# Optimization experiments

Hardware: AMD Instinct MI355X
Metric: run time of the kernel (lower is better)

Reference implementation:

```python
import jax, jax.numpy as jnp
import numpy as np

N_NODES = 50000
N_EDGES = 800000
D_FEAT = 128


def setup_inputs() -> dict:
    key = jax.random.key(0)
    k1, k2, k3 = jax.random.split(key, 3)
    x = jax.random.normal(k1, (N_NODES, D_FEAT), dtype=jnp.float32)
    edge_index = jax.random.randint(k2, (2, N_EDGES), 0, N_NODES, dtype=jnp.int64)
    eps = jnp.zeros((1,), dtype=jnp.float32)  # trainable eps, init 0
    p = jax.random.uniform(k3, (1,), dtype=jnp.float32, minval=-1.0, maxval=1.0)
    return {"x": x, "edge_index": edge_index, "eps": eps, "p": p}


def reference(x, edge_index, eps, p):
    # x: [N, d]; edge_index: [2, E] with (row, col)
    row, col = edge_index[0], edge_index[1]
    n = x.shape[0]

    # symmetric-ish GCN norm (degree computed over col only, as in source)
    deg = jax.ops.segment_sum(jnp.ones_like(col, dtype=x.dtype), col, num_segments=n)
    deg_inv_sqrt = jnp.where(deg > 0, deg ** -0.5, 0.0)
    norm = deg_inv_sqrt[row] * deg_inv_sqrt[col]  # [E]

    # nonlinear aggregation branch
    pp = jax.nn.sigmoid(p) * 2.0  # scalar in (0, 2)
    scale = pp * x  # [N, d]
    softmax = jnp.exp(scale - scale.max())  # global-max-stabilized exp

    sm_col = softmax[col]  # [E, d] gather
    deg_div = jax.ops.segment_sum(sm_col * norm[:, None], row, num_segments=n)  # [N, d]
    weights = sm_col / (deg_div[row] + 1e-6)  # [E, d]

    agg = jax.ops.segment_sum(weights * x[col] * norm[:, None], row, num_segments=n)  # [N, d]
    out = agg + (1.0 + eps) * x
    return out
```

## Files before the change

### kernel.cpp

```cpp
#include <hip/hip_runtime.h>
#include <hip/hip_fp16.h>
#include <math.h>

#define N_NODES 50000
#define N_EDGES 800000
#define D_FEAT 128

#define BSHIFT 6
#define BNODES 64
#define NBUCK ((N_NODES + BNODES - 1) / BNODES)
#define BCAP 1280
#define SLOT_CAP 64

#define PART_BLOCKS 256
#define PART_CHUNK (N_EDGES / PART_BLOCKS)

typedef __attribute__((ext_vector_type(4))) _Float16 half4;

__global__ void __launch_bounds__(256) k_cvtmax(const float* __restrict__ x,
                                                half4* __restrict__ x16,
                                                float* __restrict__ partials) {
    const float4* x4 = (const float4*)x;
    const int total4 = N_NODES * D_FEAT / 4;
    float m = -INFINITY;
    for (int i = blockIdx.x * blockDim.x + threadIdx.x; i < total4; i += gridDim.x * blockDim.x) {
        float4 v = x4[i];
        m = fmaxf(m, fmaxf(fmaxf(v.x, v.y), fmaxf(v.z, v.w)));
        half4 h;
        h.x = (_Float16)v.x; h.y = (_Float16)v.y; h.z = (_Float16)v.z; h.w = (_Float16)v.w;
        x16[i] = h;
    }
    for (int off = 32; off > 0; off >>= 1)
        m = fmaxf(m, __shfl_down(m, off, 64));
    __shared__ float smem[4];
    int lane = threadIdx.x & 63, wid = threadIdx.x >> 6;
    if (lane == 0) smem[wid] = m;
    __syncthreads();
    if (threadIdx.x == 0)
        partials[blockIdx.x] = fmaxf(fmaxf(smem[0], smem[1]), fmaxf(smem[2], smem[3]));
}

__global__ void __launch_bounds__(256) k_max2(const float* __restrict__ partials,
                                              float* __restrict__ maxval) {
    float m = fmaxf(partials[threadIdx.x], partials[threadIdx.x + 256]);
    for (int off = 32; off > 0; off >>= 1)
        m = fmaxf(m, __shfl_down(m, off, 64));
    __shared__ float smem[4];
    int lane = threadIdx.x & 63, wid = threadIdx.x >> 6;
    if (lane == 0) smem[wid] = m;
    __syncthreads();
    if (threadIdx.x == 0)
        maxval[0] = fmaxf(fmaxf(smem[0], smem[1]), fmaxf(smem[2], smem[3]));
}

__global__ void __launch_bounds__(512) k_part(const int* __restrict__ row,
                                              const int* __restrict__ col,
                                              int* __restrict__ gcur_row,
                                              int* __restrict__ gcur_col,
                                              int2* __restrict__ be_row,
                                              int* __restrict__ be_col) {
    __shared__ int h_row[NBUCK];
    __shared__ int h_col[NBUCK];
    int e0 = blockIdx.x * PART_CHUNK;
    for (int i = threadIdx.x; i < NBUCK; i += 512) { h_row[i] = 0; h_col[i] = 0; }
    __syncthreads();
    for (int e = e0 + threadIdx.x; e < e0 + PART_CHUNK; e += 512) {
        atomicAdd(&h_row[row[e] >> BSHIFT], 1);
        atomicAdd(&h_col[col[e] >> BSHIFT], 1);
    }
    __syncthreads();
    for (int i = threadIdx.x; i < NBUCK; i += 512) {
        int base_r = atomicAdd(&gcur_row[i], h_row[i]);
        h_row[i] = i * BCAP + base_r;
        int base_c = atomicAdd(&gcur_col[i], h_col[i]);
        h_col[i] = i * BCAP + base_c;
    }
    __syncthreads();
    for (int e = e0 + threadIdx.x; e < e0 + PART_CHUNK; e += 512) {
        int r = row[e], c = col[e];
        int pr = atomicAdd(&h_row[r >> BSHIFT], 1);
        if (pr < (r >> BSHIFT) * BCAP + BCAP) be_row[pr] = make_int2(r, c);
        int pc = atomicAdd(&h_col[c >> BSHIFT], 1);
        if (pc < (c >> BSHIFT) * BCAP + BCAP) be_col[pc] = c;
    }
}

__global__ void __launch_bounds__(256) k_degcol(const int* __restrict__ gcur_col,
                                                const int* __restrict__ be_col,
                                                float* __restrict__ dis) {
    __shared__ int h[BNODES];
    int b = blockIdx.x;
    if (threadIdx.x < BNODES) h[threadIdx.x] = 0;
    __syncthreads();
    int cnt = min(gcur_col[b], BCAP);
    int base = b * BCAP;
    for (int k = threadIdx.x; k < cnt; k += 256)
        atomicAdd(&h[be_col[base + k] & (BNODES - 1)], 1);
    __syncthreads();
    if (threadIdx.x < BNODES) {
        int n = (b << BSHIFT) + threadIdx.x;
        if (n < N_NODES) {
            int d = h[threadIdx.x];
            dis[n] = (d > 0) ? rsqrtf((float)d) : 0.0f;
        }
    }
}

__global__ void __launch_bounds__(512) k_agg(const half4* __restrict__ x16,
                                             const float* __restrict__ x,
                                             const int* __restrict__ gcur_row,
                                             const int2* __restrict__ be_row,
                                             const float* __restrict__ dis,
                                             const float* __restrict__ maxval,
                                             const float* __restrict__ eps_p,
                                             const float* __restrict__ p_p,
                                             float* __restrict__ out) {
    __shared__ int s_cnt[BNODES];
    __shared__ int s_slot[BNODES][SLOT_CAP];
    __shared__ float s_dis[BNODES][SLOT_CAP];
    int b = blockIdx.x;
    if (threadIdx.x < BNODES) s_cnt[threadIdx.x] = 0;
    __syncthreads();
    int ecnt = min(gcur_row[b], BCAP);
    int base = b * BCAP;
    for (int k = threadIdx.x; k < ecnt; k += 512) {
        int2 e = be_row[base + k];
        int ln = e.x & (BNODES - 1);
        int pos = atomicAdd(&s_cnt[ln], 1);
        if (pos < SLOT_CAP) {
            s_slot[ln][pos] = e.y;
            s_dis[ln][pos] = dis[e.y];
        }
    }
    __syncthreads();

    int g = threadIdx.x >> 5;
    int t = threadIdx.x & 31;
    float pp = 2.0f / (1.0f + __expf(-p_p[0]));
    float M  = pp * maxval[0];
    float ke = 1.0f + eps_p[0];
    const float4* x4 = (const float4*)x;

    for (int ln = g; ln < BNODES; ln += 16) {
        int n = (b << BSHIFT) + ln;
        if (n >= N_NODES) continue;
        int cnt = min(s_cnt[ln], SLOT_CAP);
        float dn = dis[n];
        float4 S = make_float4(0.f, 0.f, 0.f, 0.f);
        float4 T = make_float4(0.f, 0.f, 0.f, 0.f);
        #pragma unroll 4
        for (int j = 0; j < cnt; ++j) {
            int c = s_slot[ln][j];
            float nr = dn * s_dis[ln][j];
            half4 hv = x16[c * 32 + t];
            float x0 = (float)hv.x, x1 = (float)hv.y, x2 = (float)hv.z, x3 = (float)hv.w;
            float e0 = __expf(fmaf(pp, x0, -M));
            float e1 = __expf(fmaf(pp, x1, -M));
            float e2 = __expf(fmaf(pp, x2, -M));
            float e3 = __expf(fmaf(pp, x3, -M));
            float w0 = nr * e0, w1 = nr * e1, w2 = nr * e2, w3 = nr * e3;
            S.x += w0; S.y += w1; S.z += w2; S.w += w3;
            T.x = fmaf(w0, x0, T.x);
            T.y = fmaf(w1, x1, T.y);
            T.z = fmaf(w2, x2, T.z);
            T.w = fmaf(w3, x3, T.w);
        }
        float4 xn = x4[n * 32 + t];
        float4 o;
        o.x = T.x / (S.x + 1e-6f) + ke * xn.x;
        o.y = T.y / (S.y + 1e-6f) + ke * xn.y;
        o.z = T.z / (S.z + 1e-6f) + ke * xn.z;
        o.w = T.w / (S.w + 1e-6f) + ke * xn.w;
        ((float4*)out)[n * 32 + t] = o;
    }
}

extern "C" void kernel_launch(void* const* d_in, const int* in_sizes, int n_in,
                              void* d_out, int out_size, void* d_ws, size_t ws_size,
                              hipStream_t stream) {
    const float* x   = (const float*)d_in[0];
    const int*   ei  = (const int*)d_in[1];
    const float* eps = (const float*)d_in[2];
    const float* p   = (const float*)d_in[3];
    float* out = (float*)d_out;

    const int* row = ei;
    const int* col = ei + N_EDGES;

    char* ws = (char*)d_ws;
    int*   gcur_row = (int*)ws;
    int*   gcur_col = (int*)(ws + 4 * NBUCK);
    float* maxval   = (float*)(ws + 4 * 2 * NBUCK);
    float* partials = (float*)(ws + 4 * (2 * NBUCK + 1));
    float* dis      = (float*)(ws + 4 * (2 * NBUCK + 1 + 512));
    size_t off = 4 * (size_t)(2 * NBUCK + 1 + 512 + N_NODES);
    off = (off + 15) & ~(size_t)15;
    half4* x16      = (half4*)(ws + off);
    off += (size_t)N_NODES * D_FEAT * 2;
    int*   be_col   = (int*)(ws + off);
    off += (size_t)NBUCK * BCAP * 4;
    int2*  be_row   = (int2*)(ws + off);

    hipMemsetAsync(ws, 0, 4 * 2 * NBUCK, stream);

    k_cvtmax<<<512, 256, 0, stream>>>(x, x16, partials);
    k_max2<<<1, 256, 0, stream>>>(partials, maxval);
    k_part<<<PART_BLOCKS, 512, 0, stream>>>(row, col, gcur_row, gcur_col, be_row, be_col);
    k_degcol<<<NBUCK, 256, 0, stream>>>(gcur_col, be_col, dis);
    k_agg<<<NBUCK, 512, 0, stream>>>(x16, x, gcur_row, be_row, dis, maxval, eps, p, out);
}
```

Measured before the change: 169.3 us.

## Fuse all stages into one persistent cooperative kernel with grid syncs

Replaces the memset and five separate launches with a single cooperative persistent kernel. It runs convert/max, edge partitioning, column degree and aggregation as phases separated by grid.sync, with blocks looping over buckets. Counter zeroing and the final max reduction move inside the kernel. The exponent is rewritten as exp2f with log2(e) folded into the scale and max constants. This removes launch gaps and the memset, at the cost of grid-wide barriers and a grid capped at 512 blocks, which gives uneven bucket distribution in the aggregation phase. A three-kernel fallback is kept, but it zeroes the counters in the same kernel that accumulates into them, without a grid-wide barrier between the two.

```diff
diff --git a/kernel.cpp b/kernel.cpp
--- a/kernel.cpp
+++ b/kernel.cpp
@@ -1,4 +1,5 @@
 #include <hip/hip_runtime.h>
+#include <hip/hip_cooperative_groups.h>
 #include <hip/hip_fp16.h>
 #include <math.h>
 
@@ -12,71 +13,79 @@
 #define BCAP 1280
 #define SLOT_CAP 64
 
-#define PART_BLOCKS 256
-#define PART_CHUNK (N_EDGES / PART_BLOCKS)
+#define BLOCK 512
+#define MAXGRID 512
+#define PREP_GRID 512
 
 typedef __attribute__((ext_vector_type(4))) _Float16 half4;
-
-__global__ void __launch_bounds__(256) k_cvtmax(const float* __restrict__ x,
-                                                half4* __restrict__ x16,
-                                                float* __restrict__ partials) {
+namespace cg = cooperative_groups;
+
+struct SmemLayout {
+    int   cnt[BNODES];
+    float scal[4];
+    int   slot[BNODES][SLOT_CAP];
+    float dsv[BNODES][SLOT_CAP];
+};
+
+__device__ __forceinline__ void phase_cvtmax(const float* __restrict__ x,
+                                             half4* __restrict__ x16,
+                                             float* __restrict__ partials,
+                                             int* __restrict__ gcur,
+                                             SmemLayout& sm) {
+    const int tid = threadIdx.x;
+    const int gtid = blockIdx.x * BLOCK + tid;
+    if (gtid < 2 * NBUCK) gcur[gtid] = 0;
     const float4* x4 = (const float4*)x;
     const int total4 = N_NODES * D_FEAT / 4;
+    const int stride = gridDim.x * BLOCK;
     float m = -INFINITY;
-    for (int i = blockIdx.x * blockDim.x + threadIdx.x; i < total4; i += gridDim.x * blockDim.x) {
+    for (int i = gtid; i < total4; i += stride) {
         float4 v = x4[i];
         m = fmaxf(m, fmaxf(fmaxf(v.x, v.y), fmaxf(v.z, v.w)));
         half4 h;
-        h.x = (_Float16)v.x; h.y = (_Float16)v.y; h.z = (_Float16)v.z; h.w = (_Float16)v.w;
+        h.x = (_Float16)v.x; h.y = (_Float16)v.y;
+        h.z = (_Float16)v.z; h.w = (_Float16)v.w;
         x16[i] = h;
     }
     for (int off = 32; off > 0; off >>= 1)
         m = fmaxf(m, __shfl_down(m, off, 64));
-    __shared__ float smem[4];
-    int lane = threadIdx.x & 63, wid = threadIdx.x >> 6;
-    if (lane == 0) smem[wid] = m;
-    __syncthreads();
-    if (threadIdx.x == 0)
-        partials[blockIdx.x] = fmaxf(fmaxf(smem[0], smem[1]), fmaxf(smem[2], smem[3]));
-}
-
-__global__ void __launch_bounds__(256) k_max2(const float* __restrict__ partials,
-                                              float* __restrict__ maxval) {
-    float m = fmaxf(partials[threadIdx.x], partials[threadIdx.x + 256]);
-    for (int off = 32; off > 0; off >>= 1)
-        m = fmaxf(m, __shfl_down(m, off, 64));
-    __shared__ float smem[4];
-    int lane = threadIdx.x & 63, wid = threadIdx.x >> 6;
-    if (lane == 0) smem[wid] = m;
-    __syncthreads();
-    if (threadIdx.x == 0)
-        maxval[0] = fmaxf(fmaxf(smem[0], smem[1]), fmaxf(smem[2], smem[3]));
-}
-
-__global__ void __launch_bounds__(512) k_part(const int* __restrict__ row,
-                                              const int* __restrict__ col,
-                                              int* __restrict__ gcur_row,
-                                              int* __restrict__ gcur_col,
-                                              int2* __restrict__ be_row,
-                                              int* __restrict__ be_col) {
-    __shared__ int h_row[NBUCK];
-    __shared__ int h_col[NBUCK];
-    int e0 = blockIdx.x * PART_CHUNK;
-    for (int i = threadIdx.x; i < NBUCK; i += 512) { h_row[i] = 0; h_col[i] = 0; }
-    __syncthreads();
-    for (int e = e0 + threadIdx.x; e < e0 + PART_CHUNK; e += 512) {
+    float* red = (float*)sm.cnt;
+    const int lane = tid & 63, wid = tid >> 6;
+    if (lane == 0) red[wid] = m;
+    __syncthreads();
+    if (tid == 0) {
+        for (int w = 1; w < BLOCK / 64; ++w) m = fmaxf(m, red[w]);
+        partials[blockIdx.x] = m;
+    }
+    __syncthreads();
+}
+
+__device__ __forceinline__ void phase_part(const int* __restrict__ row,
+                                           const int* __restrict__ col,
+                                           int* __restrict__ gcur,
+                                           int2* __restrict__ be_row,
+                                           int* __restrict__ be_col,
+                                           SmemLayout& sm) {
+    int* h_row = (int*)sm.slot;
+    int* h_col = (int*)sm.dsv;
+    const int tid = threadIdx.x;
+    const int G = gridDim.x;
+    const int echunk = (N_EDGES + G - 1) / G;
+    const int e0 = blockIdx.x * echunk;
+    const int e1 = min(e0 + echunk, N_EDGES);
+    for (int i = tid; i < NBUCK; i += BLOCK) { h_row[i] = 0; h_col[i] = 0; }
+    __syncthreads();
+    for (int e = e0 + tid; e < e1; e += BLOCK) {
         atomicAdd(&h_row[row[e] >> BSHIFT], 1);
         atomicAdd(&h_col[col[e] >> BSHIFT], 1);
     }
     __syncthreads();
-    for (int i = threadIdx.x; i < NBUCK; i += 512) {
-        int base_r = atomicAdd(&gcur_row[i], h_row[i]);
-        h_row[i] = i * BCAP + base_r;
-        int base_c = atomicAdd(&gcur_col[i], h_col[i]);
-        h_col[i] = i * BCAP + base_c;
-    }
-    __syncthreads();
-    for (int e = e0 + threadIdx.x; e < e0 + PART_CHUNK; e += 512) {
+    for (int i = tid; i < NBUCK; i += BLOCK) {
+        h_row[i] = i * BCAP + atomicAdd(&gcur[i], h_row[i]);
+        h_col[i] = i * BCAP + atomicAdd(&gcur[NBUCK + i], h_col[i]);
+    }
+    __syncthreads();
+    for (int e = e0 + tid; e < e1; e += BLOCK) {
         int r = row[e], c = col[e];
         int pr = atomicAdd(&h_row[r >> BSHIFT], 1);
         if (pr < (r >> BSHIFT) * BCAP + BCAP) be_row[pr] = make_int2(r, c);
@@ -85,94 +94,174 @@
     }
 }
 
-__global__ void __launch_bounds__(256) k_degcol(const int* __restrict__ gcur_col,
-                                                const int* __restrict__ be_col,
-                                                float* __restrict__ dis) {
-    __shared__ int h[BNODES];
-    int b = blockIdx.x;
-    if (threadIdx.x < BNODES) h[threadIdx.x] = 0;
-    __syncthreads();
-    int cnt = min(gcur_col[b], BCAP);
-    int base = b * BCAP;
-    for (int k = threadIdx.x; k < cnt; k += 256)
-        atomicAdd(&h[be_col[base + k] & (BNODES - 1)], 1);
-    __syncthreads();
-    if (threadIdx.x < BNODES) {
-        int n = (b << BSHIFT) + threadIdx.x;
-        if (n < N_NODES) {
-            int d = h[threadIdx.x];
-            dis[n] = (d > 0) ? rsqrtf((float)d) : 0.0f;
+__device__ __forceinline__ void phase_degcol(const int* __restrict__ gcur,
+                                             const int* __restrict__ be_col,
+                                             float* __restrict__ dis,
+                                             SmemLayout& sm) {
+    const int tid = threadIdx.x;
+    for (int b = blockIdx.x; b < NBUCK; b += gridDim.x) {
+        if (tid < BNODES) sm.cnt[tid] = 0;
+        __syncthreads();
+        int cnt = min(gcur[NBUCK + b], BCAP);
+        int base = b * BCAP;
+        for (int k = tid; k < cnt; k += BLOCK)
+            atomicAdd(&sm.cnt[be_col[base + k] & (BNODES - 1)], 1);
+        __syncthreads();
+        if (tid < BNODES) {
+            int n = (b << BSHIFT) + tid;
+            if (n < N_NODES) {
+                int d0 = sm.cnt[tid];
+                dis[n] = (d0 > 0) ? rsqrtf((float)d0) : 0.0f;
+            }
         }
-    }
-}
-
-__global__ void __launch_bounds__(512) k_agg(const half4* __restrict__ x16,
-                                             const float* __restrict__ x,
-                                             const int* __restrict__ gcur_row,
-                                             const int2* __restrict__ be_row,
-                                             const float* __restrict__ dis,
-                                             const float* __restrict__ maxval,
-                                             const float* __restrict__ eps_p,
-                                             const float* __restrict__ p_p,
-                                             float* __restrict__ out) {
-    __shared__ int s_cnt[BNODES];
-    __shared__ int s_slot[BNODES][SLOT_CAP];
-    __shared__ float s_dis[BNODES][SLOT_CAP];
-    int b = blockIdx.x;
-    if (threadIdx.x < BNODES) s_cnt[threadIdx.x] = 0;
-    __syncthreads();
-    int ecnt = min(gcur_row[b], BCAP);
-    int base = b * BCAP;
-    for (int k = threadIdx.x; k < ecnt; k += 512) {
-        int2 e = be_row[base + k];
-        int ln = e.x & (BNODES - 1);
-        int pos = atomicAdd(&s_cnt[ln], 1);
-        if (pos < SLOT_CAP) {
-            s_slot[ln][pos] = e.y;
-            s_dis[ln][pos] = dis[e.y];
+        __syncthreads();
+    }
+}
+
+__device__ __forceinline__ void phase_scal(const float* __restrict__ partials,
+                                           int nparts,
+                                           const float* __restrict__ eps_p,
+                                           const float* __restrict__ p_p,
+                                           SmemLayout& sm) {
+    const int tid = threadIdx.x;
+    float m = (tid < nparts) ? partials[tid] : -INFINITY;
+    for (int off = 32; off > 0; off >>= 1)
+        m = fmaxf(m, __shfl_down(m, off, 64));
+    float* red = (float*)sm.cnt;
+    const int lane = tid & 63, wid = tid >> 6;
+    if (lane == 0) red[wid] = m;
+    __syncthreads();
+    if (tid == 0) {
+        for (int w = 1; w < BLOCK / 64; ++w) m = fmaxf(m, red[w]);
+        float pp = 2.0f / (1.0f + __expf(-p_p[0]));
+        const float LOG2E = 1.44269504f;
+        sm.scal[0] = pp * m * LOG2E;
+        sm.scal[1] = pp * LOG2E;
+        sm.scal[2] = 1.0f + eps_p[0];
+    }
+    __syncthreads();
+}
+
+__device__ __forceinline__ void phase_agg(const float* __restrict__ x,
+                                          const half4* __restrict__ x16,
+                                          const int* __restrict__ gcur,
+                                          const int2* __restrict__ be_row,
+                                          const float* __restrict__ dis,
+                                          float* __restrict__ out,
+                                          SmemLayout& sm) {
+    const int tid = threadIdx.x;
+    const float Mlg = sm.scal[0], ppl = sm.scal[1], ke = sm.scal[2];
+    const float4* x4 = (const float4*)x;
+    for (int b = blockIdx.x; b < NBUCK; b += gridDim.x) {
+        if (tid < BNODES) sm.cnt[tid] = 0;
+        __syncthreads();
+        int ecnt = min(gcur[b], BCAP);
+        int base = b * BCAP;
+        for (int k = tid; k < ecnt; k += BLOCK) {
+            int2 e = be_row[base + k];
+            int ln = e.x & (BNODES - 1);
+            int pos = atomicAdd(&sm.cnt[ln], 1);
+            if (pos < SLOT_CAP) {
+                sm.slot[ln][pos] = e.y;
+                sm.dsv[ln][pos] = dis[e.y];
+            }
         }
-    }
-    __syncthreads();
-
-    int g = threadIdx.x >> 5;
-    int t = threadIdx.x & 31;
-    float pp = 2.0f / (1.0f + __expf(-p_p[0]));
-    float M  = pp * maxval[0];
-    float ke = 1.0f + eps_p[0];
-    const float4* x4 = (const float4*)x;
-
-    for (int ln = g; ln < BNODES; ln += 16) {
-        int n = (b << BSHIFT) + ln;
-        if (n >= N_NODES) continue;
-        int cnt = min(s_cnt[ln], SLOT_CAP);
-        float dn = dis[n];
-        float4 S = make_float4(0.f, 0.f, 0.f, 0.f);
-        float4 T = make_float4(0.f, 0.f, 0.f, 0.f);
-        #pragma unroll 4
-        for (int j = 0; j < cnt; ++j) {
-            int c = s_slot[ln][j];
-            float nr = dn * s_dis[ln][j];
-            half4 hv = x16[c * 32 + t];
-            float x0 = (float)hv.x, x1 = (float)hv.y, x2 = (float)hv.z, x3 = (float)hv.w;
-            float e0 = __expf(fmaf(pp, x0, -M));
-            float e1 = __expf(fmaf(pp, x1, -M));
-            float e2 = __expf(fmaf(pp, x2, -M));
-            float e3 = __expf(fmaf(pp, x3, -M));
-            float w0 = nr * e0, w1 = nr * e1, w2 = nr * e2, w3 = nr * e3;
-            S.x += w0; S.y += w1; S.z += w2; S.w += w3;
-            T.x = fmaf(w0, x0, T.x);
-            T.y = fmaf(w1, x1, T.y);
-            T.z = fmaf(w2, x2, T.z);
-            T.w = fmaf(w3, x3, T.w);
+        __syncthreads();
+        int g = tid >> 5;
+        int t = tid & 31;
+        for (int ln = g; ln < BNODES; ln += 16) {
+            int n = (b << BSHIFT) + ln;
+            if (n >= N_NODES) continue;
+            int cnt = min(sm.cnt[ln], SLOT_CAP);
+            float dn = dis[n];
+            float4 S = make_float4(0.f, 0.f, 0.f, 0.f);
+            float4 T = make_float4(0.f, 0.f, 0.f, 0.f);
+            #pragma unroll 4
+            for (int j = 0; j < cnt; ++j) {
+                int c = sm.slot[ln][j];
+                float nr = dn * sm.dsv[ln][j];
+                half4 hv = x16[c * 32 + t];
+                float x0 = (float)hv.x, x1 = (float)hv.y;
+                float x2 = (float)hv.z, x3 = (float)hv.w;
+                float e0 = exp2f(fmaf(ppl, x0, -Mlg));
+                float e1 = exp2f(fmaf(ppl, x1, -Mlg));
+                float e2 = exp2f(fmaf(ppl, x2, -Mlg));
+                float e3 = exp2f(fmaf(ppl, x3, -Mlg));
+                float w0 = nr * e0, w1 = nr * e1, w2 = nr * e2, w3 = nr * e3;
+                S.x += w0; S.y += w1; S.z += w2; S.w += w3;
+                T.x = fmaf(w0, x0, T.x);
+                T.y = fmaf(w1, x1, T.y);
+                T.z = fmaf(w2, x2, T.z);
+                T.w = fmaf(w3, x3, T.w);
+            }
+            float4 xn = x4[n * 32 + t];
+            float4 o;
+            o.x = T.x / (S.x + 1e-6f) + ke * xn.x;
+            o.y = T.y / (S.y + 1e-6f) + ke * xn.y;
+            o.z = T.z / (S.z + 1e-6f) + ke * xn.z;
+            o.w = T.w / (S.w + 1e-6f) + ke * xn.w;
+            ((float4*)out)[n * 32 + t] = o;
         }
-        float4 xn = x4[n * 32 + t];
-        float4 o;
-        o.x = T.x / (S.x + 1e-6f) + ke * xn.x;
-        o.y = T.y / (S.y + 1e-6f) + ke * xn.y;
-        o.z = T.z / (S.z + 1e-6f) + ke * xn.z;
-        o.w = T.w / (S.w + 1e-6f) + ke * xn.w;
-        ((float4*)out)[n * 32 + t] = o;
-    }
+        __syncthreads();
+    }
+}
+
+__global__ void __launch_bounds__(BLOCK, 4) k_fused(
+    const float* __restrict__ x,
+    const int* __restrict__ row,
+    const int* __restrict__ col,
+    const float* __restrict__ eps_p,
+    const float* __restrict__ p_p,
+    float* __restrict__ out,
+    half4* __restrict__ x16,
+    float* __restrict__ partials,
+    int* __restrict__ gcur,
+    int2* __restrict__ be_row,
+    int* __restrict__ be_col,
+    float* __restrict__ dis)
+{
+    cg::grid_group grid = cg::this_grid();
+    __shared__ SmemLayout sm;
+    phase_cvtmax(x, x16, partials, gcur, sm);
+    grid.sync();
+    phase_part(row, col, gcur, be_row, be_col, sm);
+    grid.sync();
+    phase_degcol(gcur, be_col, dis, sm);
+    grid.sync();
+    phase_scal(partials, gridDim.x, eps_p, p_p, sm);
+    phase_agg(x, x16, gcur, be_row, dis, out, sm);
+}
+
+__global__ void __launch_bounds__(BLOCK) k_prep(
+    const float* __restrict__ x, const int* __restrict__ row,
+    const int* __restrict__ col, half4* __restrict__ x16,
+    float* __restrict__ partials, int* __restrict__ gcur,
+    int2* __restrict__ be_row, int* __restrict__ be_col)
+{
+    __shared__ SmemLayout sm;
+    phase_cvtmax(x, x16, partials, gcur, sm);
+    __syncthreads();
+    phase_part(row, col, gcur, be_row, be_col, sm);
+}
+
+__global__ void __launch_bounds__(BLOCK) k_deg(
+    const int* __restrict__ gcur, const int* __restrict__ be_col,
+    float* __restrict__ dis)
+{
+    __shared__ SmemLayout sm;
+    phase_degcol(gcur, be_col, dis, sm);
+}
+
+__global__ void __launch_bounds__(BLOCK) k_aggk(
+    const float* __restrict__ x, const half4* __restrict__ x16,
+    const float* __restrict__ partials, int nparts,
+    const float* __restrict__ eps_p, const float* __restrict__ p_p,
+    const int* __restrict__ gcur, const int2* __restrict__ be_row,
+    const float* __restrict__ dis, float* __restrict__ out)
+{
+    __shared__ SmemLayout sm;
+    phase_scal(partials, nparts, eps_p, p_p, sm);
+    phase_agg(x, x16, gcur, be_row, dis, out, sm);
 }
 
 extern "C" void kernel_launch(void* const* d_in, const int* in_sizes, int n_in,
@@ -188,12 +277,10 @@
     const int* col = ei + N_EDGES;
 
     char* ws = (char*)d_ws;
-    int*   gcur_row = (int*)ws;
-    int*   gcur_col = (int*)(ws + 4 * NBUCK);
-    float* maxval   = (float*)(ws + 4 * 2 * NBUCK);
-    float* partials = (float*)(ws + 4 * (2 * NBUCK + 1));
-    float* dis      = (float*)(ws + 4 * (2 * NBUCK + 1 + 512));
-    size_t off = 4 * (size_t)(2 * NBUCK + 1 + 512 + N_NODES);
+    int*   gcur     = (int*)ws;
+    float* partials = (float*)(ws + 4 * 2 * NBUCK);
+    float* dis      = (float*)(ws + 4 * (2 * NBUCK + MAXGRID));
+    size_t off = 4 * (size_t)(2 * NBUCK + MAXGRID + N_NODES);
     off = (off + 15) & ~(size_t)15;
     half4* x16      = (half4*)(ws + off);
     off += (size_t)N_NODES * D_FEAT * 2;
@@ -201,11 +288,24 @@
     off += (size_t)NBUCK * BCAP * 4;
     int2*  be_row   = (int2*)(ws + off);
 
-    hipMemsetAsync(ws, 0, 4 * 2 * NBUCK, stream);
-
-    k_cvtmax<<<512, 256, 0, stream>>>(x, x16, partials);
-    k_max2<<<1, 256, 0, stream>>>(partials, maxval);
-    k_part<<<PART_BLOCKS, 512, 0, stream>>>(row, col, gcur_row, gcur_col, be_row, be_col);
-    k_degcol<<<NBUCK, 256, 0, stream>>>(gcur_col, be_col, dis);
-    k_agg<<<NBUCK, 512, 0, stream>>>(x16, x, gcur_row, be_row, dis, maxval, eps, p, out);
-}
+    int maxB = 0;
+    hipError_t oe = hipOccupancyMaxActiveBlocksPerMultiprocessor(&maxB, k_fused, BLOCK, 0);
+    bool coop_done = false;
+    if (oe == hipSuccess && maxB > 0) {
+        int g = maxB * 256;
+        if (g > MAXGRID) g = MAXGRID;
+        void* args[] = { (void*)&x, (void*)&row, (void*)&col, (void*)&eps, (void*)&p,
+                         (void*)&out, (void*)&x16, (void*)&partials, (void*)&gcur,
+                         (void*)&be_row, (void*)&be_col, (void*)&dis };
+        hipError_t le = hipLaunchCooperativeKernel((const void*)k_fused, dim3(g),
+                                                   dim3(BLOCK), args, 0, stream);
+        coop_done = (le == hipSuccess);
+    }
+    if (!coop_done) {
+        k_prep<<<PREP_GRID, BLOCK, 0, stream>>>(x, row, col, x16, partials, gcur,
+                                                be_row, be_col);
+        k_deg<<<NBUCK, BLOCK, 0, stream>>>(gcur, be_col, dis);
+        k_aggk<<<NBUCK, BLOCK, 0, stream>>>(x, x16, partials, PREP_GRID, eps, p,
+                                            gcur, be_row, dis, out);
+    }
+}
```

New measurement: 327.3 us. 93.3% more time.

## Fuse conversion/max into partition kernel, fold max reduction into aggregation, shrink buckets

Applied to the files above, without the earlier changes.

Merges the fp16 conversion and max-partial kernel with the edge partition kernel, and moves the final max reduction into each aggregation block. This removes two kernel launches. Bucket size drops from 64 to 32 nodes with 256-thread aggregation blocks and a higher occupancy hint, giving more, smaller blocks. The exponential is rewritten as exp2f with log2e prescaled. The trade-offs are redundant per-block max reduction and more buckets in the shared histograms of the partition phase.

```diff
diff --git a/kernel.cpp b/kernel.cpp
--- a/kernel.cpp
+++ b/kernel.cpp
@@ -6,77 +6,67 @@
 #define N_EDGES 800000
 #define D_FEAT 128
 
-#define BSHIFT 6
-#define BNODES 64
+#define BSHIFT 5
+#define BNODES 32
 #define NBUCK ((N_NODES + BNODES - 1) / BNODES)
-#define BCAP 1280
+#define BCAP 704
 #define SLOT_CAP 64
 
-#define PART_BLOCKS 256
-#define PART_CHUNK (N_EDGES / PART_BLOCKS)
+#define PREP_GRID 256
+#define PREP_BLOCK 512
+#define PREP_CHUNK (N_EDGES / PREP_GRID)
+#define AGG_BLOCK 256
 
 typedef __attribute__((ext_vector_type(4))) _Float16 half4;
 
-__global__ void __launch_bounds__(256) k_cvtmax(const float* __restrict__ x,
-                                                half4* __restrict__ x16,
-                                                float* __restrict__ partials) {
-    const float4* x4 = (const float4*)x;
-    const int total4 = N_NODES * D_FEAT / 4;
-    float m = -INFINITY;
-    for (int i = blockIdx.x * blockDim.x + threadIdx.x; i < total4; i += gridDim.x * blockDim.x) {
-        float4 v = x4[i];
-        m = fmaxf(m, fmaxf(fmaxf(v.x, v.y), fmaxf(v.z, v.w)));
-        half4 h;
-        h.x = (_Float16)v.x; h.y = (_Float16)v.y; h.z = (_Float16)v.z; h.w = (_Float16)v.w;
-        x16[i] = h;
-    }
-    for (int off = 32; off > 0; off >>= 1)
-        m = fmaxf(m, __shfl_down(m, off, 64));
-    __shared__ float smem[4];
-    int lane = threadIdx.x & 63, wid = threadIdx.x >> 6;
-    if (lane == 0) smem[wid] = m;
-    __syncthreads();
-    if (threadIdx.x == 0)
-        partials[blockIdx.x] = fmaxf(fmaxf(smem[0], smem[1]), fmaxf(smem[2], smem[3]));
-}
-
-__global__ void __launch_bounds__(256) k_max2(const float* __restrict__ partials,
-                                              float* __restrict__ maxval) {
-    float m = fmaxf(partials[threadIdx.x], partials[threadIdx.x + 256]);
-    for (int off = 32; off > 0; off >>= 1)
-        m = fmaxf(m, __shfl_down(m, off, 64));
-    __shared__ float smem[4];
-    int lane = threadIdx.x & 63, wid = threadIdx.x >> 6;
-    if (lane == 0) smem[wid] = m;
-    __syncthreads();
-    if (threadIdx.x == 0)
-        maxval[0] = fmaxf(fmaxf(smem[0], smem[1]), fmaxf(smem[2], smem[3]));
-}
-
-__global__ void __launch_bounds__(512) k_part(const int* __restrict__ row,
-                                              const int* __restrict__ col,
-                                              int* __restrict__ gcur_row,
-                                              int* __restrict__ gcur_col,
-                                              int2* __restrict__ be_row,
-                                              int* __restrict__ be_col) {
+__global__ void __launch_bounds__(PREP_BLOCK) k_prep(
+    const float* __restrict__ x, const int* __restrict__ row,
+    const int* __restrict__ col, half4* __restrict__ x16,
+    float* __restrict__ partials, int* __restrict__ gcur,
+    int2* __restrict__ be_row, int* __restrict__ be_col)
+{
     __shared__ int h_row[NBUCK];
     __shared__ int h_col[NBUCK];
-    int e0 = blockIdx.x * PART_CHUNK;
-    for (int i = threadIdx.x; i < NBUCK; i += 512) { h_row[i] = 0; h_col[i] = 0; }
-    __syncthreads();
-    for (int e = e0 + threadIdx.x; e < e0 + PART_CHUNK; e += 512) {
+    __shared__ float red[PREP_BLOCK / 64];
+    const int tid = threadIdx.x;
+
+    {
+        const float4* x4 = (const float4*)x;
+        const int total4 = N_NODES * D_FEAT / 4;
+        float m = -INFINITY;
+        for (int i = blockIdx.x * PREP_BLOCK + tid; i < total4; i += PREP_GRID * PREP_BLOCK) {
+            float4 v = x4[i];
+            m = fmaxf(m, fmaxf(fmaxf(v.x, v.y), fmaxf(v.z, v.w)));
+            half4 h;
+            h.x = (_Float16)v.x; h.y = (_Float16)v.y;
+            h.z = (_Float16)v.z; h.w = (_Float16)v.w;
+            x16[i] = h;
+        }
+        for (int off = 32; off > 0; off >>= 1)
+            m = fmaxf(m, __shfl_down(m, off, 64));
+        if ((tid & 63) == 0) red[tid >> 6] = m;
+        __syncthreads();
+        if (tid == 0) {
+            for (int w = 1; w < PREP_BLOCK / 64; ++w) m = fmaxf(m, red[w]);
+            partials[blockIdx.x] = m;
+        }
+    }
+
+    for (int i = tid; i < NBUCK; i += PREP_BLOCK) { h_row[i] = 0; h_col[i] = 0; }
+    __syncthreads();
+    const int e0 = blockIdx.x * PREP_CHUNK;
+    const int e1 = e0 + PREP_CHUNK;
+    for (int e = e0 + tid; e < e1; e += PREP_BLOCK) {
         atomicAdd(&h_row[row[e] >> BSHIFT], 1);
         atomicAdd(&h_col[col[e] >> BSHIFT], 1);
     }
     __syncthreads();
-    for (int i = threadIdx.x; i < NBUCK; i += 512) {
-        int base_r = atomicAdd(&gcur_row[i], h_row[i]);
-        h_row[i] = i * BCAP + base_r;
-        int base_c = atomicAdd(&gcur_col[i], h_col[i]);
-        h_col[i] = i * BCAP + base_c;
-    }
-    __syncthreads();
-    for (int e = e0 + threadIdx.x; e < e0 + PART_CHUNK; e += 512) {
+    for (int i = tid; i < NBUCK; i += PREP_BLOCK) {
+        h_row[i] = i * BCAP + atomicAdd(&gcur[i], h_row[i]);
+        h_col[i] = i * BCAP + atomicAdd(&gcur[NBUCK + i], h_col[i]);
+    }
+    __syncthreads();
+    for (int e = e0 + tid; e < e1; e += PREP_BLOCK) {
         int r = row[e], c = col[e];
         int pr = atomicAdd(&h_row[r >> BSHIFT], 1);
         if (pr < (r >> BSHIFT) * BCAP + BCAP) be_row[pr] = make_int2(r, c);
@@ -85,45 +75,65 @@
     }
 }
 
-__global__ void __launch_bounds__(256) k_degcol(const int* __restrict__ gcur_col,
-                                                const int* __restrict__ be_col,
-                                                float* __restrict__ dis) {
-    __shared__ int h[BNODES];
-    int b = blockIdx.x;
-    if (threadIdx.x < BNODES) h[threadIdx.x] = 0;
-    __syncthreads();
-    int cnt = min(gcur_col[b], BCAP);
+__global__ void __launch_bounds__(AGG_BLOCK) k_deg(
+    const int* __restrict__ gcur, const int* __restrict__ be_col,
+    float* __restrict__ dis)
+{
+    __shared__ int hcnt[BNODES];
+    const int b = blockIdx.x;
+    if (threadIdx.x < BNODES) hcnt[threadIdx.x] = 0;
+    __syncthreads();
+    int cnt = min(gcur[NBUCK + b], BCAP);
     int base = b * BCAP;
-    for (int k = threadIdx.x; k < cnt; k += 256)
-        atomicAdd(&h[be_col[base + k] & (BNODES - 1)], 1);
+    for (int k = threadIdx.x; k < cnt; k += AGG_BLOCK)
+        atomicAdd(&hcnt[be_col[base + k] & (BNODES - 1)], 1);
     __syncthreads();
     if (threadIdx.x < BNODES) {
         int n = (b << BSHIFT) + threadIdx.x;
         if (n < N_NODES) {
-            int d = h[threadIdx.x];
+            int d = hcnt[threadIdx.x];
             dis[n] = (d > 0) ? rsqrtf((float)d) : 0.0f;
         }
     }
 }
 
-__global__ void __launch_bounds__(512) k_agg(const half4* __restrict__ x16,
-                                             const float* __restrict__ x,
-                                             const int* __restrict__ gcur_row,
-                                             const int2* __restrict__ be_row,
-                                             const float* __restrict__ dis,
-                                             const float* __restrict__ maxval,
-                                             const float* __restrict__ eps_p,
-                                             const float* __restrict__ p_p,
-                                             float* __restrict__ out) {
+__global__ void __launch_bounds__(AGG_BLOCK, 8) k_agg(
+    const float* __restrict__ x, const half4* __restrict__ x16,
+    const float* __restrict__ partials,
+    const float* __restrict__ eps_p, const float* __restrict__ p_p,
+    const int* __restrict__ gcur, const int2* __restrict__ be_row,
+    const float* __restrict__ dis, float* __restrict__ out)
+{
     __shared__ int s_cnt[BNODES];
     __shared__ int s_slot[BNODES][SLOT_CAP];
     __shared__ float s_dis[BNODES][SLOT_CAP];
-    int b = blockIdx.x;
-    if (threadIdx.x < BNODES) s_cnt[threadIdx.x] = 0;
-    __syncthreads();
-    int ecnt = min(gcur_row[b], BCAP);
+    __shared__ float s_scal[4];
+    __shared__ float red[AGG_BLOCK / 64];
+    const int tid = threadIdx.x;
+
+    {
+        float m = partials[tid];
+        for (int off = 32; off > 0; off >>= 1)
+            m = fmaxf(m, __shfl_down(m, off, 64));
+        if ((tid & 63) == 0) red[tid >> 6] = m;
+        if (tid < BNODES) s_cnt[tid] = 0;
+        __syncthreads();
+        if (tid == 0) {
+            for (int w = 1; w < AGG_BLOCK / 64; ++w) m = fmaxf(m, red[w]);
+            float pp = 2.0f / (1.0f + __expf(-p_p[0]));
+            const float LOG2E = 1.44269504f;
+            s_scal[0] = pp * m * LOG2E;
+            s_scal[1] = pp * LOG2E;
+            s_scal[2] = 1.0f + eps_p[0];
+        }
+        __syncthreads();
+    }
+    const float Mlg = s_scal[0], ppl = s_scal[1], ke = s_scal[2];
+
+    const int b = blockIdx.x;
+    int ecnt = min(gcur[b], BCAP);
     int base = b * BCAP;
-    for (int k = threadIdx.x; k < ecnt; k += 512) {
+    for (int k = tid; k < ecnt; k += AGG_BLOCK) {
         int2 e = be_row[base + k];
         int ln = e.x & (BNODES - 1);
         int pos = atomicAdd(&s_cnt[ln], 1);
@@ -134,14 +144,9 @@
     }
     __syncthreads();
 
-    int g = threadIdx.x >> 5;
-    int t = threadIdx.x & 31;
-    float pp = 2.0f / (1.0f + __expf(-p_p[0]));
-    float M  = pp * maxval[0];
-    float ke = 1.0f + eps_p[0];
+    const int g = tid >> 5, t = tid & 31;
     const float4* x4 = (const float4*)x;
-
-    for (int ln = g; ln < BNODES; ln += 16) {
+    for (int ln = g; ln < BNODES; ln += AGG_BLOCK / 32) {
         int n = (b << BSHIFT) + ln;
         if (n >= N_NODES) continue;
         int cnt = min(s_cnt[ln], SLOT_CAP);
@@ -153,11 +158,12 @@
             int c = s_slot[ln][j];
             float nr = dn * s_dis[ln][j];
             half4 hv = x16[c * 32 + t];
-            float x0 = (float)hv.x, x1 = (float)hv.y, x2 = (float)hv.z, x3 = (float)hv.w;
-            float e0 = __expf(fmaf(pp, x0, -M));
-            float e1 = __expf(fmaf(pp, x1, -M));
-            float e2 = __expf(fmaf(pp, x2, -M));
-            float e3 = __expf(fmaf(pp, x3, -M));
+            float x0 = (float)hv.x, x1 = (float)hv.y;
+            float x2 = (float)hv.z, x3 = (float)hv.w;
+            float e0 = exp2f(fmaf(ppl, x0, -Mlg));
+            float e1 = exp2f(fmaf(ppl, x1, -Mlg));
+            float e2 = exp2f(fmaf(ppl, x2, -Mlg));
+            float e3 = exp2f(fmaf(ppl, x3, -Mlg));
             float w0 = nr * e0, w1 = nr * e1, w2 = nr * e2, w3 = nr * e3;
             S.x += w0; S.y += w1; S.z += w2; S.w += w3;
             T.x = fmaf(w0, x0, T.x);
@@ -188,24 +194,22 @@
     const int* col = ei + N_EDGES;
 
     char* ws = (char*)d_ws;
-    int*   gcur_row = (int*)ws;
-    int*   gcur_col = (int*)(ws + 4 * NBUCK);
-    float* maxval   = (float*)(ws + 4 * 2 * NBUCK);
-    float* partials = (float*)(ws + 4 * (2 * NBUCK + 1));
-    float* dis      = (float*)(ws + 4 * (2 * NBUCK + 1 + 512));
-    size_t off = 4 * (size_t)(2 * NBUCK + 1 + 512 + N_NODES);
+    int*   gcur     = (int*)ws;
+    float* partials = (float*)(ws + 4 * 2 * NBUCK);
+    float* dis      = (float*)(ws + 4 * (2 * NBUCK + 256));
+    size_t off = 4 * (size_t)(2 * NBUCK + 256 + N_NODES);
     off = (off + 15) & ~(size_t)15;
     half4* x16      = (half4*)(ws + off);
     off += (size_t)N_NODES * D_FEAT * 2;
     int*   be_col   = (int*)(ws + off);
     off += (size_t)NBUCK * BCAP * 4;
+    off = (off + 7) & ~(size_t)7;
     int2*  be_row   = (int2*)(ws + off);
 
-    hipMemsetAsync(ws, 0, 4 * 2 * NBUCK, stream);
-
-    k_cvtmax<<<512, 256, 0, stream>>>(x, x16, partials);
-    k_max2<<<1, 256, 0, stream>>>(partials, maxval);
-    k_part<<<PART_BLOCKS, 512, 0, stream>>>(row, col, gcur_row, gcur_col, be_row, be_col);
-    k_degcol<<<NBUCK, 256, 0, stream>>>(gcur_col, be_col, dis);
-    k_agg<<<NBUCK, 512, 0, stream>>>(x16, x, gcur_row, be_row, dis, maxval, eps, p, out);
-}
+    hipMemsetAsync(gcur, 0, 4 * 2 * NBUCK, stream);
+    k_prep<<<PREP_GRID, PREP_BLOCK, 0, stream>>>(x, row, col, x16, partials, gcur,
+                                                 be_row, be_col);
+    k_deg<<<NBUCK, AGG_BLOCK, 0, stream>>>(gcur, be_col, dis);
+    k_agg<<<NBUCK, AGG_BLOCK, 0, stream>>>(x, x16, partials, eps, p,
+                                           gcur, be_row, dis, out);
+}
```

New measurement: 177.6 us. +4.9%, slower.
